# Performance work log

Hardware: AMD Instinct MI355X
Metric: run time of the kernel (lower is better)

## Reference

```python
import jax, jax.numpy as jnp
import numpy as np

# QuadFittingFromFlow: per-pixel quadratic least-squares fit from flow.
# The CUDA extension source is unavailable; this reference implements the
# standard per-pixel quadratic cost-surface fit it describes:
#  1. for each pixel p, bilinearly sample feat1 at p + flow + (ox,oy) for the
#     3x3 offset grid (ox,oy in {-1,0,1}) and compute the SSD matching cost
#     against feat0(p)  -> 9 cost samples c_k per pixel.
#  2. fit a 2D quadratic c(x,y) ~ a x^2 + b y^2 + c xy + d x + e y + f by
#     (softmin-)weighted least squares, solving the per-pixel 6x6 normal
#     equations. Output sol = the 6 quadratic coefficients per pixel (Y,X,6).
# The 3rd flow channel (validity/confidence) does not alter the LS solution
# (uniform per-pixel rescaling of weights) and is ignored, matching the
# module's docstring that only 2 displacement channels matter.

Y, X, L = 384, 512, 32
EPS = 1e-4  # Tikhonov regularization for the 6x6 solve

# fixed 3x3 offset grid and quadratic design matrix A (9 samples x 6 coeffs)
_oy, _ox = np.meshgrid(np.arange(-1, 2), np.arange(-1, 2), indexing='ij')
OFFS_X = jnp.asarray(_ox.reshape(-1), dtype=jnp.float32)  # (9,)
OFFS_Y = jnp.asarray(_oy.reshape(-1), dtype=jnp.float32)  # (9,)
_A = np.stack([_ox.reshape(-1) ** 2, _oy.reshape(-1) ** 2,
               _ox.reshape(-1) * _oy.reshape(-1),
               _ox.reshape(-1), _oy.reshape(-1),
               np.ones(9)], axis=1).astype(np.float32)
A_DESIGN = jnp.asarray(_A)  # (9, 6)


def _bilinear(feat, px, py):
    # feat: (Y,X,L); px,py: (Y,X,9) fractional sample coords -> (Y,X,9,L)
    Yd, Xd, _ = feat.shape
    x0f, y0f = jnp.floor(px), jnp.floor(py)
    wx = (px - x0f)[..., None]
    wy = (py - y0f)[..., None]
    x0 = jnp.clip(x0f.astype(jnp.int32), 0, Xd - 1)
    x1 = jnp.clip(x0 + 1, 0, Xd - 1)
    y0 = jnp.clip(y0f.astype(jnp.int32), 0, Yd - 1)
    y1 = jnp.clip(y0 + 1, 0, Yd - 1)
    f00 = feat[y0, x0]
    f01 = feat[y0, x1]
    f10 = feat[y1, x0]
    f11 = feat[y1, x1]
    return (f00 * (1 - wx) * (1 - wy) + f01 * wx * (1 - wy)
            + f10 * (1 - wx) * wy + f11 * wx * wy)


def _quadfit(t_feat0, t_feat1, t_flow):
    Yd, Xd, _ = t_feat0.shape
    u, v = t_flow[..., 0], t_flow[..., 1]  # displacement channels
    gy, gx = jnp.meshgrid(jnp.arange(Yd, dtype=jnp.float32),
                          jnp.arange(Xd, dtype=jnp.float32), indexing='ij')
    px = gx[..., None] + u[..., None] + OFFS_X  # (Y,X,9)
    py = gy[..., None] + v[..., None] + OFFS_Y
    samp = _bilinear(t_feat1, px, py)           # (Y,X,9,L)
    c = jnp.sum((t_feat0[:, :, None, :] - samp) ** 2, axis=-1)  # (Y,X,9)
    w = jax.nn.softmax(-c, axis=-1)             # robust per-pixel weights
    AtWA = jnp.einsum('ki,yxk,kj->yxij', A_DESIGN, w, A_DESIGN) \
        + EPS * jnp.eye(6, dtype=t_feat0.dtype)  # (Y,X,6,6)
    rhs = jnp.einsum('ki,yxk->yxi', A_DESIGN, w * c)  # (Y,X,6)
    sol = jnp.linalg.solve(AtWA, rhs[..., None])[..., 0]
    return sol  # (Y,X,6)


def setup_inputs() -> dict:
    key = jax.random.key(0)
    k0, k1, k2 = jax.random.split(key, 3)
    t_feat0 = jax.random.normal(k0, (Y, X, L), dtype=jnp.float32)
    t_feat1 = jax.random.normal(k1, (Y, X, L), dtype=jnp.float32)
    t_flow = jax.random.normal(k2, (Y, X, 3), dtype=jnp.float32) * 2.0
    return {"t_feat0": t_feat0, "t_feat1": t_feat1, "t_flow": t_flow}


def reference(t_feat0, t_feat1, t_flow):
    return _quadfit(t_feat0, t_feat1, t_flow)
```

## Files before the change

kernel.cpp:

```cpp
#include <hip/hip_runtime.h>
#include <math.h>

#define Ydim 384
#define Xdim 512
#define NPIX (Ydim * Xdim)
#define EPS 1e-4

__global__ __launch_bounds__(256) void qf_cost_kernel(
    const float* __restrict__ feat0,
    const float* __restrict__ feat1,
    const float* __restrict__ flow,
    float* __restrict__ cost)
{
    int tid = blockIdx.x * blockDim.x + threadIdx.x;
    int pix = tid >> 3;
    int sub = tid & 7;
    if (pix >= NPIX) return;
    int y = pix >> 9;
    int x = pix & (Xdim - 1);

    float u = flow[pix * 3 + 0];
    float v = flow[pix * 3 + 1];
    const float4 f0 = *(const float4*)(feat0 + (size_t)pix * 32 + sub * 4);

    float pxc = (float)x + u;
    float pyc = (float)y + v;

    int   coff0[3], coff1[3];
    float wx[3];
#pragma unroll
    for (int j = 0; j < 3; ++j) {
        float px = pxc + (float)(j - 1);
        float fx = floorf(px);
        wx[j] = px - fx;
        int xi = (int)fx;
        xi = min(max(xi, 0), Xdim - 1);
        coff0[j] = xi * 32 + sub * 4;
        coff1[j] = min(xi + 1, Xdim - 1) * 32 + sub * 4;
    }

    float cacc[9];
#pragma unroll
    for (int i = 0; i < 3; ++i) {
        float py = pyc + (float)(i - 1);
        float fy = floorf(py);
        float wyv = py - fy;
        int yi = (int)fy;
        yi = min(max(yi, 0), Ydim - 1);
        int rb0 = yi * (Xdim * 32);
        int rb1 = min(yi + 1, Ydim - 1) * (Xdim * 32);
        float omwy = 1.f - wyv;
#pragma unroll
        for (int j = 0; j < 3; ++j) {
            const float4 f00 = *(const float4*)(feat1 + rb0 + coff0[j]);
            const float4 f01 = *(const float4*)(feat1 + rb0 + coff1[j]);
            const float4 f10 = *(const float4*)(feat1 + rb1 + coff0[j]);
            const float4 f11 = *(const float4*)(feat1 + rb1 + coff1[j]);
            float wxv = wx[j], omwx = 1.f - wxv;
            float w00 = omwx * omwy, w01 = wxv * omwy;
            float w10 = omwx * wyv,  w11 = wxv * wyv;
            float dx = f0.x - (f00.x * w00 + f01.x * w01 + f10.x * w10 + f11.x * w11);
            float dy = f0.y - (f00.y * w00 + f01.y * w01 + f10.y * w10 + f11.y * w11);
            float dz = f0.z - (f00.z * w00 + f01.z * w01 + f10.z * w10 + f11.z * w11);
            float dw = f0.w - (f00.w * w00 + f01.w * w01 + f10.w * w10 + f11.w * w11);
            cacc[i * 3 + j] = dx * dx + dy * dy + dz * dz + dw * dw;
        }
    }

#pragma unroll
    for (int m = 1; m <= 4; m <<= 1) {
#pragma unroll
        for (int k = 0; k < 9; ++k)
            cacc[k] += __shfl_xor(cacc[k], m);
    }
    if (sub == 0) {
#pragma unroll
        for (int k = 0; k < 9; ++k)
            cost[(size_t)pix * 9 + k] = cacc[k];
    }
}

__global__ __launch_bounds__(256) void qf_solve_kernel(
    const float* __restrict__ cost,
    float* __restrict__ out)
{
    int pix = blockIdx.x * blockDim.x + threadIdx.x;
    if (pix >= NPIX) return;

    float c[9];
#pragma unroll
    for (int k = 0; k < 9; ++k) c[k] = cost[(size_t)pix * 9 + k];

    float cmin = c[0];
#pragma unroll
    for (int k = 1; k < 9; ++k) cmin = fminf(cmin, c[k]);

    float e[9], sumf = 0.f;
#pragma unroll
    for (int k = 0; k < 9; ++k) {
        e[k] = expf(cmin - c[k]);
        sumf += e[k];
    }
    double invs = 1.0 / (double)sumf;

    double w[9], q[9];
#pragma unroll
    for (int k = 0; k < 9; ++k) {
        w[k] = (double)e[k] * invs;
        q[k] = w[k] * (double)c[k];
    }

    double sc0 = w[0] + w[3] + w[6], sc2 = w[2] + w[5] + w[8];
    double sr0 = w[0] + w[1] + w[2], sr2 = w[6] + w[7] + w[8];
    double S10 = sc2 - sc0, S20 = sc2 + sc0;
    double S01 = sr2 - sr0, S02 = sr2 + sr0;
    double S11 = (w[0] + w[8]) - (w[2] + w[6]);
    double S21 = (w[6] + w[8]) - (w[0] + w[2]);
    double S12 = (w[2] + w[8]) - (w[0] + w[6]);
    double S22 = w[0] + w[2] + w[6] + w[8];
    double S00 = sr0 + w[3] + w[4] + w[5] + sr2;

    double qc0 = q[0] + q[3] + q[6], qc2 = q[2] + q[5] + q[8];
    double qr0 = q[0] + q[1] + q[2], qr2 = q[6] + q[7] + q[8];
    double T10 = qc2 - qc0, T20 = qc2 + qc0;
    double T01 = qr2 - qr0, T02 = qr2 + qr0;
    double T11 = (q[0] + q[8]) - (q[2] + q[6]);
    double T00 = qr0 + q[3] + q[4] + q[5] + qr2;

    double M[6][6], rhs[6], ip[6];
    M[0][0] = S20 + EPS; M[0][1] = S22; M[0][2] = S11; M[0][3] = S10; M[0][4] = S21; M[0][5] = S20;
    M[1][1] = S02 + EPS; M[1][2] = S11; M[1][3] = S12; M[1][4] = S01; M[1][5] = S02;
    M[2][2] = S22 + EPS; M[2][3] = S21; M[2][4] = S12; M[2][5] = S11;
    M[3][3] = S20 + EPS; M[3][4] = S11; M[3][5] = S10;
    M[4][4] = S02 + EPS; M[4][5] = S01;
    M[5][5] = S00 + EPS;
    rhs[0] = T20; rhs[1] = T02; rhs[2] = T11; rhs[3] = T10; rhs[4] = T01; rhs[5] = T00;

#pragma unroll
    for (int p = 0; p < 6; ++p) {
        ip[p] = 1.0 / M[p][p];
#pragma unroll
        for (int r = p + 1; r < 6; ++r) {
            double f = M[p][r] * ip[p];
#pragma unroll
            for (int cc = r; cc < 6; ++cc)
                M[r][cc] -= f * M[p][cc];
            rhs[r] -= f * rhs[p];
        }
    }
    double sol[6];
#pragma unroll
    for (int p = 5; p >= 0; --p) {
        double s2 = rhs[p];
#pragma unroll
        for (int cc = p + 1; cc < 6; ++cc) s2 -= M[p][cc] * sol[cc];
        sol[p] = s2 * ip[p];
    }

#pragma unroll
    for (int i = 0; i < 6; ++i) out[(size_t)pix * 6 + i] = (float)sol[i];
}

extern "C" void kernel_launch(void* const* d_in, const int* in_sizes, int n_in,
                              void* d_out, int out_size, void* d_ws, size_t ws_size,
                              hipStream_t stream) {
    const float* feat0 = (const float*)d_in[0];
    const float* feat1 = (const float*)d_in[1];
    const float* flow  = (const float*)d_in[2];
    float* out  = (float*)d_out;
    float* cost = (float*)d_ws;

    qf_cost_kernel<<<dim3(NPIX * 8 / 256), dim3(256), 0, stream>>>(feat0, feat1, flow, cost);
    qf_solve_kernel<<<dim3((NPIX + 255) / 256), dim3(256), 0, stream>>>(cost, out);
}
```

Baseline: 116.1 us.

## Fuse cost and solve kernels, share bilinear taps, cut fp64 work

Merges the cost and solve kernels into one launch, passing the 9 costs per pixel through LDS so the workspace round trip and second launch go away. When the 3x3 sample grid is unclipped, a fast path loads a 4x4 grid of feat1 taps once instead of 36 separate loads. The softmax weights and moment sums now use float instead of double, and the fp64 reciprocal is replaced by a float rcp refined with two Newton steps. In exchange, only 32 of 256 threads do the solve after a barrier, and the lower precision may change results slightly.

```diff
diff --git a/kernel.cpp b/kernel.cpp
--- a/kernel.cpp
+++ b/kernel.cpp
@@ -6,64 +6,105 @@
 #define NPIX (Ydim * Xdim)
 #define EPS 1e-4
 
-__global__ __launch_bounds__(256) void qf_cost_kernel(
+__device__ __forceinline__ double fast_rcp64(double d) {
+    double r = (double)__builtin_amdgcn_rcpf((float)d);
+    r = r * (2.0 - d * r);
+    r = r * (2.0 - d * r);
+    return r;
+}
+
+__global__ __launch_bounds__(256) void qf_fused_kernel(
     const float* __restrict__ feat0,
     const float* __restrict__ feat1,
     const float* __restrict__ flow,
-    float* __restrict__ cost)
+    float* __restrict__ out)
 {
-    int tid = blockIdx.x * blockDim.x + threadIdx.x;
-    int pix = tid >> 3;
-    int sub = tid & 7;
-    if (pix >= NPIX) return;
-    int y = pix >> 9;
-    int x = pix & (Xdim - 1);
-
-    float u = flow[pix * 3 + 0];
-    float v = flow[pix * 3 + 1];
+    __shared__ float cost_lds[32 * 9];
+
+    const int t   = threadIdx.x;
+    const int g   = t >> 3;
+    const int sub = t & 7;
+    const int pix = blockIdx.x * 32 + g;
+    const int y = pix >> 9;
+    const int x = pix & (Xdim - 1);
+
+    const float u = flow[pix * 3 + 0];
+    const float v = flow[pix * 3 + 1];
     const float4 f0 = *(const float4*)(feat0 + (size_t)pix * 32 + sub * 4);
 
-    float pxc = (float)x + u;
-    float pyc = (float)y + v;
-
-    int   coff0[3], coff1[3];
-    float wx[3];
+    const float pxc = (float)x + u;
+    const float pyc = (float)y + v;
+
+    int   c0[3], c1[3], r0[3], r1[3];
+    float wx[3], wy[3];
 #pragma unroll
     for (int j = 0; j < 3; ++j) {
         float px = pxc + (float)(j - 1);
         float fx = floorf(px);
         wx[j] = px - fx;
-        int xi = (int)fx;
-        xi = min(max(xi, 0), Xdim - 1);
-        coff0[j] = xi * 32 + sub * 4;
-        coff1[j] = min(xi + 1, Xdim - 1) * 32 + sub * 4;
+        int xi = min(max((int)fx, 0), Xdim - 1);
+        c0[j] = xi;
+        c1[j] = min(xi + 1, Xdim - 1);
+        float py = pyc + (float)(j - 1);
+        float fy = floorf(py);
+        wy[j] = py - fy;
+        int yi = min(max((int)fy, 0), Ydim - 1);
+        r0[j] = yi;
+        r1[j] = min(yi + 1, Ydim - 1);
     }
 
     float cacc[9];
-#pragma unroll
-    for (int i = 0; i < 3; ++i) {
-        float py = pyc + (float)(i - 1);
-        float fy = floorf(py);
-        float wyv = py - fy;
-        int yi = (int)fy;
-        yi = min(max(yi, 0), Ydim - 1);
-        int rb0 = yi * (Xdim * 32);
-        int rb1 = min(yi + 1, Ydim - 1) * (Xdim * 32);
-        float omwy = 1.f - wyv;
-#pragma unroll
-        for (int j = 0; j < 3; ++j) {
-            const float4 f00 = *(const float4*)(feat1 + rb0 + coff0[j]);
-            const float4 f01 = *(const float4*)(feat1 + rb0 + coff1[j]);
-            const float4 f10 = *(const float4*)(feat1 + rb1 + coff0[j]);
-            const float4 f11 = *(const float4*)(feat1 + rb1 + coff1[j]);
-            float wxv = wx[j], omwx = 1.f - wxv;
-            float w00 = omwx * omwy, w01 = wxv * omwy;
-            float w10 = omwx * wyv,  w11 = wxv * wyv;
-            float dx = f0.x - (f00.x * w00 + f01.x * w01 + f10.x * w10 + f11.x * w11);
-            float dy = f0.y - (f00.y * w00 + f01.y * w01 + f10.y * w10 + f11.y * w11);
-            float dz = f0.z - (f00.z * w00 + f01.z * w01 + f10.z * w10 + f11.z * w11);
-            float dw = f0.w - (f00.w * w00 + f01.w * w01 + f10.w * w10 + f11.w * w11);
-            cacc[i * 3 + j] = dx * dx + dy * dy + dz * dz + dw * dw;
+    const bool fast = (c1[0] == c0[1]) & (c1[1] == c0[2])
+                    & (r1[0] == r0[1]) & (r1[1] == r0[2]);
+
+    if (fast) {
+        const int cols[4] = {c0[0], c0[1], c0[2], c1[2]};
+        const int rows[4] = {r0[0], r0[1], r0[2], r1[2]};
+        float4 F[4][4];
+#pragma unroll
+        for (int r = 0; r < 4; ++r) {
+            const float* rb = feat1 + ((size_t)rows[r] * Xdim) * 32 + sub * 4;
+#pragma unroll
+            for (int c = 0; c < 4; ++c)
+                F[r][c] = *(const float4*)(rb + (size_t)cols[c] * 32);
+        }
+#pragma unroll
+        for (int i = 0; i < 3; ++i) {
+            float wyv = wy[i], omwy = 1.f - wyv;
+#pragma unroll
+            for (int j = 0; j < 3; ++j) {
+                float wxv = wx[j], omwx = 1.f - wxv;
+                float w00 = omwx * omwy, w01 = wxv * omwy;
+                float w10 = omwx * wyv,  w11 = wxv * wyv;
+                float4 a = F[i][j], b = F[i][j + 1], c = F[i + 1][j], d = F[i + 1][j + 1];
+                float dx = f0.x - (a.x * w00 + b.x * w01 + c.x * w10 + d.x * w11);
+                float dy = f0.y - (a.y * w00 + b.y * w01 + c.y * w10 + d.y * w11);
+                float dz = f0.z - (a.z * w00 + b.z * w01 + c.z * w10 + d.z * w11);
+                float dw = f0.w - (a.w * w00 + b.w * w01 + c.w * w10 + d.w * w11);
+                cacc[i * 3 + j] = dx * dx + dy * dy + dz * dz + dw * dw;
+            }
+        }
+    } else {
+#pragma unroll
+        for (int i = 0; i < 3; ++i) {
+            float wyv = wy[i], omwy = 1.f - wyv;
+            int rb0 = r0[i] * (Xdim * 32);
+            int rb1 = r1[i] * (Xdim * 32);
+#pragma unroll
+            for (int j = 0; j < 3; ++j) {
+                const float4 f00 = *(const float4*)(feat1 + rb0 + c0[j] * 32 + sub * 4);
+                const float4 f01 = *(const float4*)(feat1 + rb0 + c1[j] * 32 + sub * 4);
+                const float4 f10 = *(const float4*)(feat1 + rb1 + c0[j] * 32 + sub * 4);
+                const float4 f11 = *(const float4*)(feat1 + rb1 + c1[j] * 32 + sub * 4);
+                float wxv = wx[j], omwx = 1.f - wxv;
+                float w00 = omwx * omwy, w01 = wxv * omwy;
+                float w10 = omwx * wyv,  w11 = wxv * wyv;
+                float dx = f0.x - (f00.x * w00 + f01.x * w01 + f10.x * w10 + f11.x * w11);
+                float dy = f0.y - (f00.y * w00 + f01.y * w01 + f10.y * w10 + f11.y * w11);
+                float dz = f0.z - (f00.z * w00 + f01.z * w01 + f10.z * w10 + f11.z * w11);
+                float dw = f0.w - (f00.w * w00 + f01.w * w01 + f10.w * w10 + f11.w * w11);
+                cacc[i * 3 + j] = dx * dx + dy * dy + dz * dz + dw * dw;
+            }
         }
     }
 
@@ -76,20 +117,15 @@
     if (sub == 0) {
 #pragma unroll
         for (int k = 0; k < 9; ++k)
-            cost[(size_t)pix * 9 + k] = cacc[k];
-    }
-}
-
-__global__ __launch_bounds__(256) void qf_solve_kernel(
-    const float* __restrict__ cost,
-    float* __restrict__ out)
-{
-    int pix = blockIdx.x * blockDim.x + threadIdx.x;
-    if (pix >= NPIX) return;
+            cost_lds[g * 9 + k] = cacc[k];
+    }
+    __syncthreads();
+
+    if (t >= 32) return;
 
     float c[9];
 #pragma unroll
-    for (int k = 0; k < 9; ++k) c[k] = cost[(size_t)pix * 9 + k];
+    for (int k = 0; k < 9; ++k) c[k] = cost_lds[t * 9 + k];
 
     float cmin = c[0];
 #pragma unroll
@@ -101,44 +137,44 @@
         e[k] = expf(cmin - c[k]);
         sumf += e[k];
     }
-    double invs = 1.0 / (double)sumf;
-
-    double w[9], q[9];
+    float invs = 1.f / sumf;
+
+    float w[9], q[9];
 #pragma unroll
     for (int k = 0; k < 9; ++k) {
-        w[k] = (double)e[k] * invs;
-        q[k] = w[k] * (double)c[k];
-    }
-
-    double sc0 = w[0] + w[3] + w[6], sc2 = w[2] + w[5] + w[8];
-    double sr0 = w[0] + w[1] + w[2], sr2 = w[6] + w[7] + w[8];
-    double S10 = sc2 - sc0, S20 = sc2 + sc0;
-    double S01 = sr2 - sr0, S02 = sr2 + sr0;
-    double S11 = (w[0] + w[8]) - (w[2] + w[6]);
-    double S21 = (w[6] + w[8]) - (w[0] + w[2]);
-    double S12 = (w[2] + w[8]) - (w[0] + w[6]);
-    double S22 = w[0] + w[2] + w[6] + w[8];
-    double S00 = sr0 + w[3] + w[4] + w[5] + sr2;
-
-    double qc0 = q[0] + q[3] + q[6], qc2 = q[2] + q[5] + q[8];
-    double qr0 = q[0] + q[1] + q[2], qr2 = q[6] + q[7] + q[8];
-    double T10 = qc2 - qc0, T20 = qc2 + qc0;
-    double T01 = qr2 - qr0, T02 = qr2 + qr0;
-    double T11 = (q[0] + q[8]) - (q[2] + q[6]);
-    double T00 = qr0 + q[3] + q[4] + q[5] + qr2;
+        w[k] = e[k] * invs;
+        q[k] = w[k] * c[k];
+    }
+
+    float sc0 = w[0] + w[3] + w[6], sc2 = w[2] + w[5] + w[8];
+    float sr0 = w[0] + w[1] + w[2], sr2 = w[6] + w[7] + w[8];
+    float S10 = sc2 - sc0, S20 = sc2 + sc0;
+    float S01 = sr2 - sr0, S02 = sr2 + sr0;
+    float S11 = (w[0] + w[8]) - (w[2] + w[6]);
+    float S21 = (w[6] + w[8]) - (w[0] + w[2]);
+    float S12 = (w[2] + w[8]) - (w[0] + w[6]);
+    float S22 = w[0] + w[2] + w[6] + w[8];
+    float S00 = sr0 + w[3] + w[4] + w[5] + sr2;
+
+    float qc0 = q[0] + q[3] + q[6], qc2 = q[2] + q[5] + q[8];
+    float qr0 = q[0] + q[1] + q[2], qr2 = q[6] + q[7] + q[8];
+    float T10 = qc2 - qc0, T20 = qc2 + qc0;
+    float T01 = qr2 - qr0, T02 = qr2 + qr0;
+    float T11 = (q[0] + q[8]) - (q[2] + q[6]);
+    float T00 = qr0 + q[3] + q[4] + q[5] + qr2;
 
     double M[6][6], rhs[6], ip[6];
-    M[0][0] = S20 + EPS; M[0][1] = S22; M[0][2] = S11; M[0][3] = S10; M[0][4] = S21; M[0][5] = S20;
-    M[1][1] = S02 + EPS; M[1][2] = S11; M[1][3] = S12; M[1][4] = S01; M[1][5] = S02;
-    M[2][2] = S22 + EPS; M[2][3] = S21; M[2][4] = S12; M[2][5] = S11;
-    M[3][3] = S20 + EPS; M[3][4] = S11; M[3][5] = S10;
-    M[4][4] = S02 + EPS; M[4][5] = S01;
-    M[5][5] = S00 + EPS;
+    M[0][0] = (double)S20 + EPS; M[0][1] = S22; M[0][2] = S11; M[0][3] = S10; M[0][4] = S21; M[0][5] = S20;
+    M[1][1] = (double)S02 + EPS; M[1][2] = S11; M[1][3] = S12; M[1][4] = S01; M[1][5] = S02;
+    M[2][2] = (double)S22 + EPS; M[2][3] = S21; M[2][4] = S12; M[2][5] = S11;
+    M[3][3] = (double)S20 + EPS; M[3][4] = S11; M[3][5] = S10;
+    M[4][4] = (double)S02 + EPS; M[4][5] = S01;
+    M[5][5] = (double)S00 + EPS;
     rhs[0] = T20; rhs[1] = T02; rhs[2] = T11; rhs[3] = T10; rhs[4] = T01; rhs[5] = T00;
 
 #pragma unroll
     for (int p = 0; p < 6; ++p) {
-        ip[p] = 1.0 / M[p][p];
+        ip[p] = fast_rcp64(M[p][p]);
 #pragma unroll
         for (int r = p + 1; r < 6; ++r) {
             double f = M[p][r] * ip[p];
@@ -157,8 +193,9 @@
         sol[p] = s2 * ip[p];
     }
 
-#pragma unroll
-    for (int i = 0; i < 6; ++i) out[(size_t)pix * 6 + i] = (float)sol[i];
+    const int opix = blockIdx.x * 32 + t;
+#pragma unroll
+    for (int i = 0; i < 6; ++i) out[(size_t)opix * 6 + i] = (float)sol[i];
 }
 
 extern "C" void kernel_launch(void* const* d_in, const int* in_sizes, int n_in,
@@ -167,9 +204,7 @@
     const float* feat0 = (const float*)d_in[0];
     const float* feat1 = (const float*)d_in[1];
     const float* flow  = (const float*)d_in[2];
-    float* out  = (float*)d_out;
-    float* cost = (float*)d_ws;
-
-    qf_cost_kernel<<<dim3(NPIX * 8 / 256), dim3(256), 0, stream>>>(feat0, feat1, flow, cost);
-    qf_solve_kernel<<<dim3((NPIX + 255) / 256), dim3(256), 0, stream>>>(cost, out);
+    float* out = (float*)d_out;
+
+    qf_fused_kernel<<<dim3(NPIX / 32), dim3(256), 0, stream>>>(feat0, feat1, flow, out);
 }
```

New measurement: 109.6 us. 5.6% less time.
